# Optimization experiments

Hardware: AMD Instinct MI355X
Metric: run time of the kernel (lower is better)

Reference implementation:

```python
import jax, jax.numpy as jnp
import numpy as np

# module hyperparams (init_kwargs)
L = 8
K = 32
TEMP = 0.1
# problem sizes
D, NG, DIM = 64, 256, 512   # D groups, NG rows per group, feature dim
N = 65536                   # negative candidate pool size (g0.shape[0])
P = D - L                   # number of positive pairs (i, i+L)
EPS = 1e-8                  # torch F.cosine_similarity eps


def _cos(a, b, axis):
    # torch-style cosine: dot / (max(||a||,eps) * max(||b||,eps))
    na = jnp.maximum(jnp.sqrt(jnp.sum(a * a, axis=axis)), EPS)
    nb = jnp.maximum(jnp.sqrt(jnp.sum(b * b, axis=axis)), EPS)
    return jnp.sum(a * b, axis=axis) / (na * nb)


def setup_inputs() -> dict:
    key = jax.random.key(0)
    k1, k2, k3, k4, k5, k6 = jax.random.split(key, 6)
    embs = jax.random.normal(k1, (D, NG, DIM), dtype=jnp.float32)
    g0 = jax.random.normal(k2, (N, DIM), dtype=jnp.float32)
    g1 = jax.random.normal(k3, (N, DIM), dtype=jnp.float32)
    g2 = jax.random.normal(k4, (N, DIM), dtype=jnp.float32)
    neg1 = jax.random.randint(k5, (P, K), 0, N)  # stand-in for per-pair randperm(N)[:K]
    neg2 = jax.random.randint(k6, (P, K), 0, N)
    return {"embs": embs, "g0": g0, "g1": g1, "g2": g2, "neg1": neg1, "neg2": neg2}


def reference(embs, g0, g1, g2, neg1, neg2):
    # per-group sum vectors (torch: sum_list). NOTE: sum_neg_list / sample_tensors
    # in the original are dead code on the hard_neg=True output path.
    sums = embs.sum(axis=1)                       # [D, DIM]
    ii = jnp.arange(P)
    jj = ii + L
    s_i = sums[ii]                                # [P, DIM], grads flow
    s_j = jax.lax.stop_gradient(sums[jj])         # detached in both pos terms
    pos = _cos(s_i, s_j, axis=-1)                 # [P]

    a = g1[neg1]                                  # [P, K, DIM]
    b = g2[neg2]                                  # [P, K, DIM]
    # torch cosine_similarity default dim=1 on [1,K,DIM] vs [K,DIM] -> cosine over K
    sim_neg = _cos(a, b, axis=1)                  # [P, DIM]

    num = jnp.exp(pos / TEMP)                     # [P]
    den = num + jnp.exp(sim_neg / TEMP).sum(axis=1)
    loss_i = -jnp.log(num / den)                  # [P]
    # loss_j is numerically identical (cosine is symmetric, same detach pattern)
    total = 2.0 * loss_i.sum()
    return total
```

## Files before the change

### kernel.cpp

```cpp
#include <hip/hip_runtime.h>
#include <math.h>

#define DGROUPS 64
#define NG      256
#define DIM     512
#define LPAR    8
#define KNEG    32
#define PPAIRS  (DGROUPS - LPAR)
#define NCHUNKS 8
#define CHUNK   (NG / NCHUNKS)
#define CEPS    1e-8f
#define INV_T   10.0f

#define WS_POS_OFF 262144
#define WS_EN_OFF  262208

__global__ void k_sum_partial(const float* __restrict__ embs,
                              float* __restrict__ partial) {
    const int b = blockIdx.x;
    const int d = b >> 3;
    const int c = b & 7;
    const int t = threadIdx.x;
    const float4* src = (const float4*)(embs + (size_t)d * NG * DIM);
    float4 acc = make_float4(0.f, 0.f, 0.f, 0.f);
    int idx = (c * CHUNK) * (DIM / 4) + t;
    #pragma unroll 4
    for (int n = 0; n < CHUNK; ++n) {
        float4 v = src[idx];
        acc.x += v.x; acc.y += v.y; acc.z += v.z; acc.w += v.w;
        idx += DIM / 4;
    }
    ((float4*)(partial + (size_t)b * DIM))[t] = acc;
}

__global__ void k_pos(const float* __restrict__ partial,
                      float* __restrict__ pos) {
    const int p = blockIdx.x;
    const int t = threadIdx.x;
    float4 si = make_float4(0.f, 0.f, 0.f, 0.f);
    float4 sj = make_float4(0.f, 0.f, 0.f, 0.f);
    #pragma unroll
    for (int c = 0; c < NCHUNKS; ++c) {
        float4 a = ((const float4*)(partial + (size_t)(p * NCHUNKS + c) * DIM))[t];
        float4 b = ((const float4*)(partial + (size_t)((p + LPAR) * NCHUNKS + c) * DIM))[t];
        si.x += a.x; si.y += a.y; si.z += a.z; si.w += a.w;
        sj.x += b.x; sj.y += b.y; sj.z += b.z; sj.w += b.w;
    }
    float dot = si.x * sj.x + si.y * sj.y + si.z * sj.z + si.w * sj.w;
    float na  = si.x * si.x + si.y * si.y + si.z * si.z + si.w * si.w;
    float nb  = sj.x * sj.x + sj.y * sj.y + sj.z * sj.z + sj.w * sj.w;

    #pragma unroll
    for (int off = 32; off >= 1; off >>= 1) {
        dot += __shfl_down(dot, off, 64);
        na  += __shfl_down(na,  off, 64);
        nb  += __shfl_down(nb,  off, 64);
    }
    __shared__ float red[3][2];
    const int wave = t >> 6, lane = t & 63;
    if (lane == 0) { red[0][wave] = dot; red[1][wave] = na; red[2][wave] = nb; }
    __syncthreads();
    if (t == 0) {
        dot = red[0][0] + red[0][1];
        na  = red[1][0] + red[1][1];
        nb  = red[2][0] + red[2][1];
        pos[p] = dot / (fmaxf(sqrtf(na), CEPS) * fmaxf(sqrtf(nb), CEPS));
    }
}

__global__ void k_neg(const float* __restrict__ g1, const float* __restrict__ g2,
                      const int* __restrict__ neg1, const int* __restrict__ neg2,
                      float* __restrict__ en) {
    const int p = blockIdx.x;
    const int t = threadIdx.x;
    __shared__ int i1[KNEG], i2[KNEG];
    if (t < KNEG)            i1[t] = neg1[p * KNEG + t];
    else if (t < 2 * KNEG)   i2[t - KNEG] = neg2[p * KNEG + (t - KNEG)];
    __syncthreads();

    float sab = 0.f, saa = 0.f, sbb = 0.f;
    #pragma unroll 8
    for (int k = 0; k < KNEG; ++k) {
        float a = g1[(size_t)i1[k] * DIM + t];
        float b = g2[(size_t)i2[k] * DIM + t];
        sab += a * b; saa += a * a; sbb += b * b;
    }
    float sim = sab / (fmaxf(sqrtf(saa), CEPS) * fmaxf(sqrtf(sbb), CEPS));
    float e = expf(sim * INV_T);

    #pragma unroll
    for (int off = 32; off >= 1; off >>= 1)
        e += __shfl_down(e, off, 64);
    __shared__ float red[8];
    const int wave = t >> 6, lane = t & 63;
    if (lane == 0) red[wave] = e;
    __syncthreads();
    if (t == 0) {
        float s = 0.f;
        #pragma unroll
        for (int w = 0; w < 8; ++w) s += red[w];
        en[p] = s;
    }
}

__global__ void k_final(const float* __restrict__ pos, const float* __restrict__ en,
                        float* __restrict__ out) {
    const int t = threadIdx.x;
    float l = 0.f;
    if (t < PPAIRS) {
        float pp  = pos[t] * INV_T;
        float num = expf(pp);
        l = logf(num + en[t]) - pp;
    }
    #pragma unroll
    for (int off = 32; off >= 1; off >>= 1)
        l += __shfl_down(l, off, 64);
    if (t == 0) out[0] = 2.0f * l;
}

extern "C" void kernel_launch(void* const* d_in, const int* in_sizes, int n_in,
                              void* d_out, int out_size, void* d_ws, size_t ws_size,
                              hipStream_t stream) {
    const float* embs = (const float*)d_in[0];
    const float* g1   = (const float*)d_in[2];
    const float* g2   = (const float*)d_in[3];
    const int*   neg1 = (const int*)d_in[4];
    const int*   neg2 = (const int*)d_in[5];
    float* ws  = (float*)d_ws;
    float* out = (float*)d_out;

    float* partial = ws;
    float* pos     = ws + WS_POS_OFF;
    float* en      = ws + WS_EN_OFF;

    k_sum_partial<<<DGROUPS * NCHUNKS, 128, 0, stream>>>(embs, partial);
    k_pos<<<PPAIRS, 128, 0, stream>>>(partial, pos);
    k_neg<<<PPAIRS, 512, 0, stream>>>(g1, g2, neg1, neg2, en);
    k_final<<<1, 64, 0, stream>>>(pos, en, out);
}
```

Baseline: 19.83 us.

## Fuse four kernels into two with last-block atomic reduction

Merges the group-sum and negative-similarity kernels into one launch by splitting block indices, and merges the positive-cosine and final-loss kernels using an atomic ticket counter so the last block does the final reduction. It also doubles the chunk count for the embedding sum and switches the negative gather to float4 with 128 threads. The aim is to remove launch overhead and inter-kernel gaps for a tiny, launch-bound workload. In exchange it adds atomic traffic, a counter reset that relies on stream ordering, and fewer threads per negative block.

New measurement: 20.99 us. 5.9% more time.

```diff
diff --git a/kernel.cpp b/kernel.cpp
--- a/kernel.cpp
+++ b/kernel.cpp
@@ -7,48 +7,93 @@
 #define LPAR    8
 #define KNEG    32
 #define PPAIRS  (DGROUPS - LPAR)
-#define NCHUNKS 8
+#define NCHUNKS 16
 #define CHUNK   (NG / NCHUNKS)
 #define CEPS    1e-8f
 #define INV_T   10.0f
 
-#define WS_POS_OFF 262144
-#define WS_EN_OFF  262208
+#define NB_A    (DGROUPS * NCHUNKS)
+#define NB_K1   (NB_A + PPAIRS)
 
-__global__ void k_sum_partial(const float* __restrict__ embs,
-                              float* __restrict__ partial) {
-    const int b = blockIdx.x;
-    const int d = b >> 3;
-    const int c = b & 7;
-    const int t = threadIdx.x;
-    const float4* src = (const float4*)(embs + (size_t)d * NG * DIM);
-    float4 acc = make_float4(0.f, 0.f, 0.f, 0.f);
-    int idx = (c * CHUNK) * (DIM / 4) + t;
-    #pragma unroll 4
-    for (int n = 0; n < CHUNK; ++n) {
-        float4 v = src[idx];
-        acc.x += v.x; acc.y += v.y; acc.z += v.z; acc.w += v.w;
-        idx += DIM / 4;
-    }
-    ((float4*)(partial + (size_t)b * DIM))[t] = acc;
+#define WS_EN   (NB_A * DIM)
+#define WS_LOSS (WS_EN + 64)
+#define WS_CNT  (WS_LOSS + 64)
+
+__device__ __forceinline__ void f4acc(float4& a, const float4 v) {
+    a.x += v.x; a.y += v.y; a.z += v.z; a.w += v.w;
 }
 
-__global__ void k_pos(const float* __restrict__ partial,
-                      float* __restrict__ pos) {
+__global__ void k1_fused(const float* __restrict__ embs,
+                         const float* __restrict__ g1, const float* __restrict__ g2,
+                         const int* __restrict__ neg1, const int* __restrict__ neg2,
+                         float* __restrict__ ws) {
+    const int b = blockIdx.x;
+    const int t = threadIdx.x;
+
+    if (b < NB_A) {
+        const int d = b >> 4;
+        const int c = b & 15;
+        const float4* src = (const float4*)(embs + (size_t)d * NG * DIM);
+        float4 acc = make_float4(0.f, 0.f, 0.f, 0.f);
+        int idx = (c * CHUNK) * (DIM / 4) + t;
+        #pragma unroll
+        for (int n = 0; n < CHUNK; ++n) {
+            f4acc(acc, src[idx]);
+            idx += DIM / 4;
+        }
+        ((float4*)(ws + (size_t)b * DIM))[t] = acc;
+    } else {
+        const int p = b - NB_A;
+        if (p == 0 && t == 0) ((int*)(ws + WS_CNT))[0] = 0;
+
+        __shared__ int i1[KNEG], i2[KNEG];
+        if (t < KNEG)          i1[t] = neg1[p * KNEG + t];
+        else if (t < 2 * KNEG) i2[t - KNEG] = neg2[p * KNEG + (t - KNEG)];
+        __syncthreads();
+
+        float4 sab = make_float4(0.f,0.f,0.f,0.f);
+        float4 saa = make_float4(0.f,0.f,0.f,0.f);
+        float4 sbb = make_float4(0.f,0.f,0.f,0.f);
+        #pragma unroll 8
+        for (int k = 0; k < KNEG; ++k) {
+            float4 a = ((const float4*)g1)[(size_t)i1[k] * (DIM/4) + t];
+            float4 bb = ((const float4*)g2)[(size_t)i2[k] * (DIM/4) + t];
+            sab.x += a.x*bb.x; sab.y += a.y*bb.y; sab.z += a.z*bb.z; sab.w += a.w*bb.w;
+            saa.x += a.x*a.x;  saa.y += a.y*a.y;  saa.z += a.z*a.z;  saa.w += a.w*a.w;
+            sbb.x += bb.x*bb.x; sbb.y += bb.y*bb.y; sbb.z += bb.z*bb.z; sbb.w += bb.w*bb.w;
+        }
+        float e =
+            expf(INV_T * sab.x / (fmaxf(sqrtf(saa.x), CEPS) * fmaxf(sqrtf(sbb.x), CEPS))) +
+            expf(INV_T * sab.y / (fmaxf(sqrtf(saa.y), CEPS) * fmaxf(sqrtf(sbb.y), CEPS))) +
+            expf(INV_T * sab.z / (fmaxf(sqrtf(saa.z), CEPS) * fmaxf(sqrtf(sbb.z), CEPS))) +
+            expf(INV_T * sab.w / (fmaxf(sqrtf(saa.w), CEPS) * fmaxf(sqrtf(sbb.w), CEPS)));
+
+        #pragma unroll
+        for (int off = 32; off >= 1; off >>= 1)
+            e += __shfl_down(e, off, 64);
+        __shared__ float red[2];
+        const int wave = t >> 6, lane = t & 63;
+        if (lane == 0) red[wave] = e;
+        __syncthreads();
+        if (t == 0) ws[WS_EN + p] = red[0] + red[1];
+    }
+}
+
+__global__ void k2_pos_final(const float* __restrict__ ws, float* __restrict__ ws_mut,
+                             float* __restrict__ out) {
     const int p = blockIdx.x;
     const int t = threadIdx.x;
-    float4 si = make_float4(0.f, 0.f, 0.f, 0.f);
-    float4 sj = make_float4(0.f, 0.f, 0.f, 0.f);
+
+    float4 si = make_float4(0.f,0.f,0.f,0.f);
+    float4 sj = make_float4(0.f,0.f,0.f,0.f);
     #pragma unroll
     for (int c = 0; c < NCHUNKS; ++c) {
-        float4 a = ((const float4*)(partial + (size_t)(p * NCHUNKS + c) * DIM))[t];
-        float4 b = ((const float4*)(partial + (size_t)((p + LPAR) * NCHUNKS + c) * DIM))[t];
-        si.x += a.x; si.y += a.y; si.z += a.z; si.w += a.w;
-        sj.x += b.x; sj.y += b.y; sj.z += b.z; sj.w += b.w;
+        f4acc(si, ((const float4*)ws)[(size_t)(p * NCHUNKS + c) * (DIM/4) + t]);
+        f4acc(sj, ((const float4*)ws)[(size_t)((p + LPAR) * NCHUNKS + c) * (DIM/4) + t]);
     }
-    float dot = si.x * sj.x + si.y * sj.y + si.z * sj.z + si.w * sj.w;
-    float na  = si.x * si.x + si.y * si.y + si.z * si.z + si.w * si.w;
-    float nb  = sj.x * sj.x + sj.y * sj.y + sj.z * sj.z + sj.w * sj.w;
+    float dot = si.x*sj.x + si.y*sj.y + si.z*sj.z + si.w*sj.w;
+    float na  = si.x*si.x + si.y*si.y + si.z*si.z + si.w*si.w;
+    float nb  = sj.x*sj.x + sj.y*sj.y + sj.z*sj.z + sj.w*sj.w;
 
     #pragma unroll
     for (int off = 32; off >= 1; off >>= 1) {
@@ -57,65 +102,41 @@
         nb  += __shfl_down(nb,  off, 64);
     }
     __shared__ float red[3][2];
+    __shared__ int is_last;
     const int wave = t >> 6, lane = t & 63;
     if (lane == 0) { red[0][wave] = dot; red[1][wave] = na; red[2][wave] = nb; }
-    __syncthreads();
-    if (t == 0) {
-        dot = red[0][0] + red[0][1];
-        na  = red[1][0] + red[1][1];
-        nb  = red[2][0] + red[2][1];
-        pos[p] = dot / (fmaxf(sqrtf(na), CEPS) * fmaxf(sqrtf(nb), CEPS));
-    }
-}
-
-__global__ void k_neg(const float* __restrict__ g1, const float* __restrict__ g2,
-                      const int* __restrict__ neg1, const int* __restrict__ neg2,
-                      float* __restrict__ en) {
-    const int p = blockIdx.x;
-    const int t = threadIdx.x;
-    __shared__ int i1[KNEG], i2[KNEG];
-    if (t < KNEG)            i1[t] = neg1[p * KNEG + t];
-    else if (t < 2 * KNEG)   i2[t - KNEG] = neg2[p * KNEG + (t - KNEG)];
+    if (t == 0) is_last = 0;
     __syncthreads();
 
-    float sab = 0.f, saa = 0.f, sbb = 0.f;
-    #pragma unroll 8
-    for (int k = 0; k < KNEG; ++k) {
-        float a = g1[(size_t)i1[k] * DIM + t];
-        float b = g2[(size_t)i2[k] * DIM + t];
-        sab += a * b; saa += a * a; sbb += b * b;
+    if (t == 0) {
+        float dd = red[0][0] + red[0][1];
+        float aa = red[1][0] + red[1][1];
+        float bb = red[2][0] + red[2][1];
+        float pos = dd / (fmaxf(sqrtf(aa), CEPS) * fmaxf(sqrtf(bb), CEPS));
+        float pp  = pos * INV_T;
+        float en  = ws[WS_EN + p];
+        float loss = logf(expf(pp) + en) - pp;
+        __hip_atomic_store(&ws_mut[WS_LOSS + p], loss,
+                           __ATOMIC_RELEASE, __HIP_MEMORY_SCOPE_AGENT);
+        int ticket = __hip_atomic_fetch_add((int*)(ws_mut + WS_CNT), 1,
+                                            __ATOMIC_ACQ_REL, __HIP_MEMORY_SCOPE_AGENT);
+        if (ticket == PPAIRS - 1) is_last = 1;
     }
-    float sim = sab / (fmaxf(sqrtf(saa), CEPS) * fmaxf(sqrtf(sbb), CEPS));
-    float e = expf(sim * INV_T);
+    __syncthreads();
 
-    #pragma unroll
-    for (int off = 32; off >= 1; off >>= 1)
-        e += __shfl_down(e, off, 64);
-    __shared__ float red[8];
-    const int wave = t >> 6, lane = t & 63;
-    if (lane == 0) red[wave] = e;
-    __syncthreads();
-    if (t == 0) {
-        float s = 0.f;
-        #pragma unroll
-        for (int w = 0; w < 8; ++w) s += red[w];
-        en[p] = s;
+    if (is_last) {
+        __threadfence();
+        float l = 0.f;
+        if (t < PPAIRS)
+            l = __hip_atomic_load(&ws_mut[WS_LOSS + t],
+                                  __ATOMIC_ACQUIRE, __HIP_MEMORY_SCOPE_AGENT);
+        if (t < 64) {
+            #pragma unroll
+            for (int off = 32; off >= 1; off >>= 1)
+                l += __shfl_down(l, off, 64);
+            if (t == 0) out[0] = 2.0f * l;
+        }
     }
-}
-
-__global__ void k_final(const float* __restrict__ pos, const float* __restrict__ en,
-                        float* __restrict__ out) {
-    const int t = threadIdx.x;
-    float l = 0.f;
-    if (t < PPAIRS) {
-        float pp  = pos[t] * INV_T;
-        float num = expf(pp);
-        l = logf(num + en[t]) - pp;
-    }
-    #pragma unroll
-    for (int off = 32; off >= 1; off >>= 1)
-        l += __shfl_down(l, off, 64);
-    if (t == 0) out[0] = 2.0f * l;
 }
 
 extern "C" void kernel_launch(void* const* d_in, const int* in_sizes, int n_in,
@@ -129,12 +150,6 @@
     float* ws  = (float*)d_ws;
     float* out = (float*)d_out;
 
-    float* partial = ws;
-    float* pos     = ws + WS_POS_OFF;
-    float* en      = ws + WS_EN_OFF;
-
-    k_sum_partial<<<DGROUPS * NCHUNKS, 128, 0, stream>>>(embs, partial);
-    k_pos<<<PPAIRS, 128, 0, stream>>>(partial, pos);
-    k_neg<<<PPAIRS, 512, 0, stream>>>(g1, g2, neg1, neg2, en);
-    k_final<<<1, 64, 0, stream>>>(pos, en, out);
+    k1_fused<<<NB_K1, 128, 0, stream>>>(embs, g1, g2, neg1, neg2, ws);
+    k2_pos_final<<<PPAIRS, 128, 0, stream>>>(ws, ws, out);
 }
```
